# Performance work log

Measured on AMD Instinct MI355X. Metric: run time of the kernel, lower is better.

The kernel has to match this reference:

```python
import jax, jax.numpy as jnp
import numpy as np

N_NODES = 100000

def spmm(rows, cols, vals, x):
    # out[r] = sum_e vals[e] * x[cols[e]] for edges with rows[e] == r
    msgs = vals[:, None] * x[cols]            # [E, F]
    return jax.ops.segment_sum(msgs, rows, num_segments=N_NODES)

def setup_inputs() -> dict:
    key = jax.random.key(0)
    ks = jax.random.split(key, 8)
    N, E, F_IN, H, C = N_NODES, 1600000, 128, 128, 64
    x = jax.random.normal(ks[0], (N, F_IN), dtype=jnp.float32)
    edge_rows = jax.random.randint(ks[1], (E,), 0, N, dtype=jnp.int32)
    edge_cols = jax.random.randint(ks[2], (E,), 0, N, dtype=jnp.int32)
    edge_vals = jax.random.uniform(ks[3], (E,), dtype=jnp.float32)
    W1 = jax.random.normal(ks[4], (F_IN, H), dtype=jnp.float32) * (1.0 / np.sqrt(F_IN))
    b1 = jnp.zeros((H,), dtype=jnp.float32)
    W2 = jax.random.normal(ks[5], (H, C), dtype=jnp.float32) * (1.0 / np.sqrt(H))
    b2 = jnp.zeros((C,), dtype=jnp.float32)
    return {"x": x, "edge_rows": edge_rows, "edge_cols": edge_cols,
            "edge_vals": edge_vals, "W1": W1, "b1": b1, "W2": W2, "b2": b2}

def reference(x, edge_rows, edge_cols, edge_vals, W1, b1, W2, b2):
    # Layer 1: spmm(adj, x) then linear, then ReLU (dropout = identity at eval)
    h = spmm(edge_rows, edge_cols, edge_vals, x)   # [N, F_IN]
    h = h @ W1 + b1                                # [N, H]
    h = jax.nn.relu(h)
    # Layer 2
    h = spmm(edge_rows, edge_cols, edge_vals, h)   # [N, H]
    return h @ W2 + b2                             # [N, C]
```

## Files before the change

### kernel.cpp

```cpp
#include <hip/hip_runtime.h>


typedef __attribute__((ext_vector_type(8))) short short8;
typedef __attribute__((ext_vector_type(4))) float floatx4;
typedef __attribute__((ext_vector_type(2))) float floatx2;

#define ELLS 64
#define H2LD 136
#define RW   256
#define CH   4096
#define EPT  16
#define MAXB 400

static __device__ __forceinline__ unsigned short f2bf(float f) {
    unsigned int u = __builtin_bit_cast(unsigned int, f);
    u += 0x7fffu + ((u >> 16) & 1u);
    return (unsigned short)(u >> 16);
}
static __device__ __forceinline__ float bflo(unsigned int u) {
    return __builtin_bit_cast(float, u << 16);
}
static __device__ __forceinline__ float bfhi(unsigned int u) {
    return __builtin_bit_cast(float, u & 0xffff0000u);
}
static __device__ __forceinline__ float slotval(unsigned int s) {
    return (float)(s >> 17) * (1.0f / 32767.0f);
}

__global__ __launch_bounds__(256) void prep_kernel(
    const float* __restrict__ W1, const float* __restrict__ W2,
    unsigned short* __restrict__ W1t, unsigned short* __restrict__ W2t)
{
    int idx = blockIdx.x * 256 + threadIdx.x;
    if (idx < 128 * 128) {
        int n = idx >> 7, k = idx & 127;
        W1t[idx] = f2bf(W1[(size_t)k * 128 + n]);
    }
    if (idx < 64 * 128) {
        int n = idx >> 7, k = idx & 127;
        W2t[idx] = f2bf(W2[(size_t)k * 64 + n]);
    }
}

static __device__ __forceinline__ void gemm1_body(
    const float* __restrict__ A, const unsigned short* __restrict__ Wt,
    unsigned short* __restrict__ Y, int N, int bid)
{
    const int lane = threadIdx.x & 63;
    const int wave = threadIdx.x >> 6;
    const int quad = lane >> 4;
    const int l16  = lane & 15;
    const int row0 = bid * 64 + wave * 16;
    int arow = row0 + l16;
    if (arow > N - 1) arow = N - 1;

    short8 af[4];
    const float* ap = A + (size_t)arow * 128 + quad * 8;
    #pragma unroll
    for (int kt = 0; kt < 4; ++kt) {
        const floatx4* p = (const floatx4*)(ap + kt * 32);
        floatx4 lo = __builtin_nontemporal_load(p);
        floatx4 hi = __builtin_nontemporal_load(p + 1);
        short8 t;
        t[0] = (short)f2bf(lo[0]); t[1] = (short)f2bf(lo[1]);
        t[2] = (short)f2bf(lo[2]); t[3] = (short)f2bf(lo[3]);
        t[4] = (short)f2bf(hi[0]); t[5] = (short)f2bf(hi[1]);
        t[6] = (short)f2bf(hi[2]); t[7] = (short)f2bf(hi[3]);
        af[kt] = t;
    }

    floatx4 acc[8];
    #pragma unroll
    for (int nt = 0; nt < 8; ++nt) acc[nt] = (floatx4){0.f, 0.f, 0.f, 0.f};

    #pragma unroll
    for (int nt = 0; nt < 8; ++nt) {
        const unsigned short* wp = Wt + (size_t)(nt * 16 + l16) * 128 + quad * 8;
        #pragma unroll
        for (int kt = 0; kt < 4; ++kt) {
            short8 bfr = *(const short8*)(wp + kt * 32);
            acc[nt] = __builtin_amdgcn_mfma_f32_16x16x32_bf16(
                af[kt], bfr, acc[nt], 0, 0, 0);
        }
    }

    #pragma unroll
    for (int nt = 0; nt < 8; ++nt) {
        int col = nt * 16 + l16;
        #pragma unroll
        for (int r = 0; r < 4; ++r) {
            int row = row0 + quad * 4 + r;
            if (row < N)
                Y[(size_t)row * 128 + col] = f2bf(acc[nt][r]);
        }
    }
}

__global__ __launch_bounds__(256) void binA_gemm1_fused(
    const int* __restrict__ erow, const int* __restrict__ ecol,
    const float* __restrict__ eval,
    uint2* __restrict__ slab, unsigned int* __restrict__ offsT,
    int E, int NC, int NB,
    const float* __restrict__ x, const unsigned short* __restrict__ W1t,
    unsigned short* __restrict__ y1b, int N)
{
    __shared__ unsigned int hist[MAXB + 1];
    __shared__ uint2 compact[CH];

    if ((int)blockIdx.x < NC) {
        const int t     = threadIdx.x;
        const int chunk = blockIdx.x;

        for (int i = t; i <= NB; i += 256) hist[i] = 0;
        __syncthreads();

        int base = chunk * CH + t * EPT;
        unsigned int w0[EPT];
        unsigned int vb[EPT];
        int bk[EPT], rk[EPT];

        if (base + EPT <= E) {
            #pragma unroll
            for (int q = 0; q < 4; ++q) {
                int4   r4 = *(const int4*)(erow + base + q * 4);
                int4   c4 = *(const int4*)(ecol + base + q * 4);
                float4 v4 = *(const float4*)(eval + base + q * 4);
                int rr[4]   = {r4.x, r4.y, r4.z, r4.w};
                int cc[4]   = {c4.x, c4.y, c4.z, c4.w};
                float vv[4] = {v4.x, v4.y, v4.z, v4.w};
                #pragma unroll
                for (int j = 0; j < 4; ++j) {
                    int i = q * 4 + j;
                    bk[i] = rr[j] >> 8;
                    w0[i] = (unsigned int)cc[j]
                          | (((unsigned int)rr[j] & (RW - 1)) << 17);
                    vb[i] = __builtin_bit_cast(unsigned int, vv[j]);
                }
            }
        } else {
            #pragma unroll
            for (int j = 0; j < EPT; ++j) {
                int e = base + j;
                if (e < E) {
                    int r = erow[e];
                    bk[j] = r >> 8;
                    w0[j] = (unsigned int)ecol[e]
                          | (((unsigned int)r & (RW - 1)) << 17);
                    vb[j] = __builtin_bit_cast(unsigned int, eval[e]);
                } else {
                    bk[j] = NB;
                    w0[j] = 0u; vb[j] = 0u;
                }
            }
        }

        #pragma unroll
        for (int j = 0; j < EPT; ++j)
            rk[j] = (int)atomicAdd(&hist[bk[j]], 1u);
        __syncthreads();

        if (t == 0) {
            unsigned int run = 0;
            for (int i = 0; i <= NB; ++i) {
                unsigned int c = hist[i];
                hist[i] = run;
                run += c;
            }
        }
        __syncthreads();

        #pragma unroll
        for (int j = 0; j < EPT; ++j) {
            unsigned int pos = hist[bk[j]] + (unsigned int)rk[j];
            uint2 e; e.x = w0[j]; e.y = vb[j];
            compact[pos] = e;
        }
        __syncthreads();

        uint2* sp = slab + (size_t)chunk * CH;
        #pragma unroll
        for (int s = 0; s < EPT; ++s)
            sp[s * 256 + t] = compact[s * 256 + t];
        unsigned int* op = offsT + (size_t)chunk * (NB + 1);
        for (int i = t; i <= NB; i += 256) op[i] = hist[i];
    } else {
        gemm1_body(x, W1t, y1b, N, blockIdx.x - NC);
    }
}

__global__ __launch_bounds__(256) void binB(
    const uint2* __restrict__ slab, const unsigned int* __restrict__ offsT,
    unsigned int* __restrict__ ell, int* __restrict__ deg,
    int NC, int NB, int N)
{
    __shared__ unsigned int ell_lds[RW * ELLS];
    __shared__ unsigned int cur[RW];

    const int t = threadIdx.x;
    const int b = blockIdx.x;

    for (int i = t; i < RW; i += 256) cur[i] = 0;
    __syncthreads();

    const int grp = t >> 5;
    const int sl  = t & 31;
    for (int cbase = 0; cbase < NC; cbase += 8) {
        int c = cbase + grp;
        if (c < NC) {
            const unsigned int* op = offsT + (size_t)c * (NB + 1) + b;
            unsigned int off = op[0];
            unsigned int end = op[1];
            const uint2* sp = slab + (size_t)c * CH;
            for (unsigned int i = off + (unsigned)sl; i < end; i += 32) {
                uint2 e = sp[i];
                unsigned int rin = e.x >> 17;
                unsigned int col = e.x & 0x1FFFFu;
                float v = __builtin_bit_cast(float, e.y);
                unsigned int q = (unsigned int)(int)(v * 32767.f + 0.5f);
                unsigned int p = atomicAdd(&cur[rin], 1u);
                if (p < ELLS)
                    ell_lds[rin * ELLS + p] = col | (q << 17);
            }
        }
    }
    __syncthreads();

    const uint4* src = (const uint4*)ell_lds;
    uint4* dst = (uint4*)(ell + (size_t)b * RW * ELLS);
    #pragma unroll
    for (int s = 0; s < (RW * ELLS / 4) / 256; ++s)
        dst[s * 256 + t] = src[s * 256 + t];

    int row = b * RW + t;
    if (row < N) deg[row] = min((int)cur[t], ELLS);
}

__global__ __launch_bounds__(1024, 8) void spmm128_gemm2_fused(
    const int* __restrict__ deg, const unsigned int* __restrict__ ell,
    const unsigned short* __restrict__ y1b, const float* __restrict__ b1,
    const unsigned short* __restrict__ W2t,
    unsigned short* __restrict__ y2b, int N)
{
    __shared__ unsigned short h2s[16 * H2LD];

    const int wave = threadIdx.x >> 6;
    const int lane = threadIdx.x & 63;
    const int row  = blockIdx.x * 16 + wave;

    unsigned int pack = 0;
    if (row < N) {
        const unsigned int* xf = (const unsigned int*)y1b;
        int d  = min(deg[row], ELLS);
        int d8 = (d + 7) & ~7;
        const unsigned int* ep = ell + ((size_t)row << 6);

        float ax[8], ay[8];
        #pragma unroll
        for (int j = 0; j < 8; ++j) { ax[j] = 0.f; ay[j] = 0.f; }

        for (int i = 0; i < d8; i += 8) {
            uint4 q0 = *(const uint4*)(ep + i);
            uint4 q1 = *(const uint4*)(ep + i + 4);
            unsigned int s[8] = {q0.x, q0.y, q0.z, q0.w,
                                 q1.x, q1.y, q1.z, q1.w};
            unsigned int sv[8];
            unsigned int u[8];
            #pragma unroll
            for (int j = 0; j < 8; ++j) {
                unsigned int ss = (i + j < d) ? s[j] : 0u;
                sv[j] = ss;
                u[j] = xf[((ss & 0x1FFFFu) << 6) | (unsigned)lane];
            }
            #pragma unroll
            for (int j = 0; j < 8; ++j) {
                float vvv = slotval(sv[j]);
                ax[j] = fmaf(vvv, bflo(u[j]), ax[j]);
                ay[j] = fmaf(vvv, bfhi(u[j]), ay[j]);
            }
        }
        float2 b = ((const float2*)b1)[lane];
        float sx = ((ax[0] + ax[1]) + (ax[2] + ax[3]))
                 + ((ax[4] + ax[5]) + (ax[6] + ax[7])) + b.x;
        float sy = ((ay[0] + ay[1]) + (ay[2] + ay[3]))
                 + ((ay[4] + ay[5]) + (ay[6] + ay[7])) + b.y;
        sx = fmaxf(sx, 0.f);
        sy = fmaxf(sy, 0.f);
        pack = (unsigned int)f2bf(sx) | ((unsigned int)f2bf(sy) << 16);
    }
    ((unsigned int*)(h2s + wave * H2LD))[lane] = pack;
    __syncthreads();

    if (wave < 4) {
        const int quad = lane >> 4;
        const int l16  = lane & 15;
        const int nt   = wave;

        short8 af[4];
        #pragma unroll
        for (int kt = 0; kt < 4; ++kt)
            af[kt] = *(const short8*)(h2s + l16 * H2LD + quad * 8 + kt * 32);

        floatx4 acc = (floatx4){0.f, 0.f, 0.f, 0.f};
        const unsigned short* wp = W2t + (size_t)(nt * 16 + l16) * 128 + quad * 8;
        #pragma unroll
        for (int kt = 0; kt < 4; ++kt) {
            short8 bfr = *(const short8*)(wp + kt * 32);
            acc = __builtin_amdgcn_mfma_f32_16x16x32_bf16(af[kt], bfr, acc, 0, 0, 0);
        }

        int col = nt * 16 + l16;
        #pragma unroll
        for (int r = 0; r < 4; ++r) {
            int grow = blockIdx.x * 16 + quad * 4 + r;
            if (grow < N)
                y2b[(size_t)grow * 64 + col] = f2bf(acc[r]);
        }
    }
}

__global__ __launch_bounds__(256) void spmm_gather64_out(
    const int* __restrict__ deg, const unsigned int* __restrict__ ell,
    const unsigned short* __restrict__ y2b,
    const float* __restrict__ bias, float* __restrict__ out, int N)
{
    int row = (blockIdx.x * 256 + threadIdx.x) >> 6;
    if (row >= N) return;
    int lane = threadIdx.x & 63;
    int half = lane >> 5, fl = lane & 31;
    const unsigned int* xf = (const unsigned int*)y2b;

    int d  = min(deg[row], ELLS);
    int d8 = (d + 7) & ~7;
    const unsigned int* ep = ell + ((size_t)row << 6);

    float ax[4], ay[4];
    #pragma unroll
    for (int j = 0; j < 4; ++j) { ax[j] = 0.f; ay[j] = 0.f; }

    for (int i = half * 4; i < d8; i += 8) {
        uint4 q = *(const uint4*)(ep + i);
        unsigned int s[4] = {q.x, q.y, q.z, q.w};
        unsigned int sv[4];
        unsigned int u[4];
        #pragma unroll
        for (int j = 0; j < 4; ++j) {
            unsigned int ss = (i + j < d) ? s[j] : 0u;
            sv[j] = ss;
            u[j] = xf[((ss & 0x1FFFFu) << 5) | (unsigned)fl];
        }
        #pragma unroll
        for (int j = 0; j < 4; ++j) {
            float vvv = slotval(sv[j]);
            ax[j] = fmaf(vvv, bflo(u[j]), ax[j]);
            ay[j] = fmaf(vvv, bfhi(u[j]), ay[j]);
        }
    }
    float sx = (ax[0] + ax[1]) + (ax[2] + ax[3]);
    float sy = (ay[0] + ay[1]) + (ay[2] + ay[3]);
    sx += __shfl_xor(sx, 32);
    sy += __shfl_xor(sy, 32);
    if (half == 0) {
        float2 b = ((const float2*)bias)[fl];
        floatx2 o; o[0] = sx + b.x; o[1] = sy + b.y;
        __builtin_nontemporal_store(o, (floatx2*)out + (size_t)row * 32 + fl);
    }
}

extern "C" void kernel_launch(void* const* d_in, const int* in_sizes, int n_in,
                              void* d_out, int out_size, void* d_ws, size_t ws_size,
                              hipStream_t stream)
{
    const float* x    = (const float*)d_in[0];
    const int*   erow = (const int*)  d_in[1];
    const int*   ecol = (const int*)  d_in[2];
    const float* eval = (const float*)d_in[3];
    const float* W1   = (const float*)d_in[4];
    const float* b1   = (const float*)d_in[5];
    const float* W2   = (const float*)d_in[6];
    const float* b2   = (const float*)d_in[7];
    float*       out  = (float*)d_out;

    const int N = in_sizes[0] / 128;
    const int E = in_sizes[1];
    const int NP = N + 64;
    const int NB = (N + RW - 1) / RW;
    const int NC = (E + CH - 1) / CH;

    unsigned short* y1b = (unsigned short*)d_ws;
    unsigned short* y2b = y1b + (size_t)NP * 128;
    unsigned short* W1t = y2b + (size_t)NP * 64;
    unsigned short* W2t = W1t + 128 * 128;
    unsigned int* ell   = (unsigned int*)(W2t + 64 * 128);
    uint2* slab         = (uint2*)(ell + (size_t)NB * RW * ELLS);
    unsigned int* offsT = (unsigned int*)(slab + (size_t)NC * CH);
    int* deg            = (int*)(offsT + (size_t)NC * (NB + 1));

    const int spmm_blocks  = (N + 3) / 4;
    const int fused_blocks = (N + 15) / 16;
    const int mfma_blocks  = (N + 63) / 64;
    const int prep_blocks  = (128 * 128 + 255) / 256;

    prep_kernel<<<prep_blocks, 256, 0, stream>>>(W1, W2, W1t, W2t);

    binA_gemm1_fused<<<NC + mfma_blocks, 256, 0, stream>>>(
        erow, ecol, eval, slab, offsT, E, NC, NB, x, W1t, y1b, N);

    binB<<<NB, 256, 0, stream>>>(slab, offsT, ell, deg, NC, NB, N);

    spmm128_gemm2_fused<<<fused_blocks, 1024, 0, stream>>>(
        deg, ell, y1b, b1, W2t, y2b, N);

    spmm_gather64_out<<<spmm_blocks, 256, 0, stream>>>(
        deg, ell, y2b, b2, out, N);
}
```

Baseline: 299.8 us.

## Slice feature matrices into 16-column panels for cache-local SpMM gathers

Stores the intermediate feature matrices in a column-sliced layout (16 bf16 columns per slice, 32 bytes per row) and splits each SpMM across slices, so each block gathers from one small panel that fits better in L2/MALL. The fused spmm+gemm2 kernel is replaced by a sliced SpMM that writes h2 to memory, a separate MFMA gemm2 kernel, and a sliced output SpMM. Edge slots are loaded once per wave and broadcast with ds_bpermute. In exchange, h2 makes an extra round trip through global memory, there is one more launch, and each gather fetches only 32 bytes per edge.

New measurement: 523.3 us. 74.6% more time.

```diff
diff --git a/kernel.cpp b/kernel.cpp
--- a/kernel.cpp
+++ b/kernel.cpp
@@ -6,7 +6,6 @@
 typedef __attribute__((ext_vector_type(2))) float floatx2;
 
 #define ELLS 64
-#define H2LD 136
 #define RW   256
 #define CH   4096
 #define EPT  16
@@ -44,7 +43,7 @@
 
 static __device__ __forceinline__ void gemm1_body(
     const float* __restrict__ A, const unsigned short* __restrict__ Wt,
-    unsigned short* __restrict__ Y, int N, int bid)
+    unsigned short* __restrict__ Ys, int NP, int N, int bid)
 {
     const int lane = threadIdx.x & 63;
     const int wave = threadIdx.x >> 6;
@@ -86,12 +85,12 @@
 
     #pragma unroll
     for (int nt = 0; nt < 8; ++nt) {
-        int col = nt * 16 + l16;
         #pragma unroll
         for (int r = 0; r < 4; ++r) {
             int row = row0 + quad * 4 + r;
             if (row < N)
-                Y[(size_t)row * 128 + col] = f2bf(acc[nt][r]);
+                Ys[(size_t)nt * NP * 16 + (size_t)row * 16 + l16] =
+                    f2bf(acc[nt][r]);
         }
     }
 }
@@ -102,7 +101,7 @@
     uint2* __restrict__ slab, unsigned int* __restrict__ offsT,
     int E, int NC, int NB,
     const float* __restrict__ x, const unsigned short* __restrict__ W1t,
-    unsigned short* __restrict__ y1b, int N)
+    unsigned short* __restrict__ y1s, int NP, int N)
 {
     __shared__ unsigned int hist[MAXB + 1];
     __shared__ uint2 compact[CH];
@@ -184,7 +183,7 @@
         unsigned int* op = offsT + (size_t)chunk * (NB + 1);
         for (int i = t; i <= NB; i += 256) op[i] = hist[i];
     } else {
-        gemm1_body(x, W1t, y1b, N, blockIdx.x - NC);
+        gemm1_body(x, W1t, y1s, NP, N, blockIdx.x - NC);
     }
 }
 
@@ -235,134 +234,139 @@
     if (row < N) deg[row] = min((int)cur[t], ELLS);
 }
 
-__global__ __launch_bounds__(1024, 8) void spmm128_gemm2_fused(
+__global__ __launch_bounds__(1024) void spmm1_sliced(
     const int* __restrict__ deg, const unsigned int* __restrict__ ell,
-    const unsigned short* __restrict__ y1b, const float* __restrict__ b1,
+    const unsigned short* __restrict__ y1s, const float* __restrict__ b1,
+    unsigned short* __restrict__ h2s, int NP, int N)
+{
+    const int slice = blockIdx.x & 7;
+    const int rblk  = blockIdx.x >> 3;
+    const int wave  = threadIdx.x >> 6;
+    const int lane  = threadIdx.x & 63;
+    const int j     = lane >> 3;
+    const int sl    = lane & 7;
+    const int row   = rblk * 16 + wave;
+    if (row >= N) return;
+
+    const unsigned int* xu = (const unsigned int*)y1s + (size_t)slice * NP * 8;
+    const unsigned int* ep = ell + ((size_t)row << 6);
+    const int d = deg[row];
+
+    unsigned int myslot = (lane < d) ? ep[lane] : 0u;
+
+    float ax = 0.f, ay = 0.f;
+    for (int i = 0; i < d; i += 8) {
+        int src = i + j;
+        unsigned int w = (unsigned int)__builtin_amdgcn_ds_bpermute(
+            src << 2, (int)myslot);
+        w = (src < d) ? w : 0u;
+        unsigned int u = xu[(w & 0x1FFFFu) * 8 + (unsigned)sl];
+        float v = slotval(w);
+        ax = fmaf(v, bflo(u), ax);
+        ay = fmaf(v, bfhi(u), ay);
+    }
+    ax += __shfl_xor(ax, 8);  ay += __shfl_xor(ay, 8);
+    ax += __shfl_xor(ax, 16); ay += __shfl_xor(ay, 16);
+    ax += __shfl_xor(ax, 32); ay += __shfl_xor(ay, 32);
+
+    if (j == 0) {
+        float2 b = ((const float2*)b1)[slice * 8 + sl];
+        float sx = fmaxf(ax + b.x, 0.f);
+        float sy = fmaxf(ay + b.y, 0.f);
+        unsigned int pk = (unsigned int)f2bf(sx)
+                        | ((unsigned int)f2bf(sy) << 16);
+        ((unsigned int*)h2s)[(size_t)slice * NP * 8 + (size_t)row * 8 + sl] = pk;
+    }
+}
+
+__global__ __launch_bounds__(256) void gemm2_kernel(
+    const unsigned short* __restrict__ h2s,
     const unsigned short* __restrict__ W2t,
-    unsigned short* __restrict__ y2b, int N)
-{
-    __shared__ unsigned short h2s[16 * H2LD];
-
+    unsigned short* __restrict__ y2s, int NP, int N)
+{
+    const int lane = threadIdx.x & 63;
     const int wave = threadIdx.x >> 6;
-    const int lane = threadIdx.x & 63;
-    const int row  = blockIdx.x * 16 + wave;
-
-    unsigned int pack = 0;
-    if (row < N) {
-        const unsigned int* xf = (const unsigned int*)y1b;
-        int d  = min(deg[row], ELLS);
-        int d8 = (d + 7) & ~7;
-        const unsigned int* ep = ell + ((size_t)row << 6);
-
-        float ax[8], ay[8];
-        #pragma unroll
-        for (int j = 0; j < 8; ++j) { ax[j] = 0.f; ay[j] = 0.f; }
-
-        for (int i = 0; i < d8; i += 8) {
-            uint4 q0 = *(const uint4*)(ep + i);
-            uint4 q1 = *(const uint4*)(ep + i + 4);
-            unsigned int s[8] = {q0.x, q0.y, q0.z, q0.w,
-                                 q1.x, q1.y, q1.z, q1.w};
-            unsigned int sv[8];
-            unsigned int u[8];
-            #pragma unroll
-            for (int j = 0; j < 8; ++j) {
-                unsigned int ss = (i + j < d) ? s[j] : 0u;
-                sv[j] = ss;
-                u[j] = xf[((ss & 0x1FFFFu) << 6) | (unsigned)lane];
-            }
-            #pragma unroll
-            for (int j = 0; j < 8; ++j) {
-                float vvv = slotval(sv[j]);
-                ax[j] = fmaf(vvv, bflo(u[j]), ax[j]);
-                ay[j] = fmaf(vvv, bfhi(u[j]), ay[j]);
-            }
-        }
-        float2 b = ((const float2*)b1)[lane];
-        float sx = ((ax[0] + ax[1]) + (ax[2] + ax[3]))
-                 + ((ax[4] + ax[5]) + (ax[6] + ax[7])) + b.x;
-        float sy = ((ay[0] + ay[1]) + (ay[2] + ay[3]))
-                 + ((ay[4] + ay[5]) + (ay[6] + ay[7])) + b.y;
-        sx = fmaxf(sx, 0.f);
-        sy = fmaxf(sy, 0.f);
-        pack = (unsigned int)f2bf(sx) | ((unsigned int)f2bf(sy) << 16);
-    }
-    ((unsigned int*)(h2s + wave * H2LD))[lane] = pack;
-    __syncthreads();
-
-    if (wave < 4) {
-        const int quad = lane >> 4;
-        const int l16  = lane & 15;
-        const int nt   = wave;
-
-        short8 af[4];
-        #pragma unroll
-        for (int kt = 0; kt < 4; ++kt)
-            af[kt] = *(const short8*)(h2s + l16 * H2LD + quad * 8 + kt * 32);
-
-        floatx4 acc = (floatx4){0.f, 0.f, 0.f, 0.f};
+    const int quad = lane >> 4;
+    const int l16  = lane & 15;
+    const int row0 = blockIdx.x * 64 + wave * 16;
+    int arow = row0 + l16;
+    if (arow > N - 1) arow = N - 1;
+
+    short8 af[4];
+    #pragma unroll
+    for (int kt = 0; kt < 4; ++kt) {
+        int slice = kt * 2 + (quad >> 1);
+        af[kt] = *(const short8*)(h2s + (size_t)slice * NP * 16
+                                  + (size_t)arow * 16 + (quad & 1) * 8);
+    }
+
+    floatx4 acc[4];
+    #pragma unroll
+    for (int nt = 0; nt < 4; ++nt) acc[nt] = (floatx4){0.f, 0.f, 0.f, 0.f};
+
+    #pragma unroll
+    for (int nt = 0; nt < 4; ++nt) {
         const unsigned short* wp = W2t + (size_t)(nt * 16 + l16) * 128 + quad * 8;
         #pragma unroll
         for (int kt = 0; kt < 4; ++kt) {
             short8 bfr = *(const short8*)(wp + kt * 32);
-            acc = __builtin_amdgcn_mfma_f32_16x16x32_bf16(af[kt], bfr, acc, 0, 0, 0);
-        }
-
-        int col = nt * 16 + l16;
+            acc[nt] = __builtin_amdgcn_mfma_f32_16x16x32_bf16(
+                af[kt], bfr, acc[nt], 0, 0, 0);
+        }
+    }
+
+    #pragma unroll
+    for (int nt = 0; nt < 4; ++nt) {
         #pragma unroll
         for (int r = 0; r < 4; ++r) {
-            int grow = blockIdx.x * 16 + quad * 4 + r;
-            if (grow < N)
-                y2b[(size_t)grow * 64 + col] = f2bf(acc[r]);
-        }
-    }
-}
-
-__global__ __launch_bounds__(256) void spmm_gather64_out(
+            int row = row0 + quad * 4 + r;
+            if (row < N)
+                y2s[(size_t)nt * NP * 16 + (size_t)row * 16 + l16] =
+                    f2bf(acc[nt][r]);
+        }
+    }
+}
+
+__global__ __launch_bounds__(1024) void spmm2_sliced(
     const int* __restrict__ deg, const unsigned int* __restrict__ ell,
-    const unsigned short* __restrict__ y2b,
-    const float* __restrict__ bias, float* __restrict__ out, int N)
-{
-    int row = (blockIdx.x * 256 + threadIdx.x) >> 6;
+    const unsigned short* __restrict__ y2s, const float* __restrict__ b2,
+    float* __restrict__ out, int NP, int N)
+{
+    const int slice = blockIdx.x & 3;
+    const int rblk  = blockIdx.x >> 2;
+    const int wave  = threadIdx.x >> 6;
+    const int lane  = threadIdx.x & 63;
+    const int j     = lane >> 3;
+    const int sl    = lane & 7;
+    const int row   = rblk * 16 + wave;
     if (row >= N) return;
-    int lane = threadIdx.x & 63;
-    int half = lane >> 5, fl = lane & 31;
-    const unsigned int* xf = (const unsigned int*)y2b;
-
-    int d  = min(deg[row], ELLS);
-    int d8 = (d + 7) & ~7;
+
+    const unsigned int* xu = (const unsigned int*)y2s + (size_t)slice * NP * 8;
     const unsigned int* ep = ell + ((size_t)row << 6);
-
-    float ax[4], ay[4];
-    #pragma unroll
-    for (int j = 0; j < 4; ++j) { ax[j] = 0.f; ay[j] = 0.f; }
-
-    for (int i = half * 4; i < d8; i += 8) {
-        uint4 q = *(const uint4*)(ep + i);
-        unsigned int s[4] = {q.x, q.y, q.z, q.w};
-        unsigned int sv[4];
-        unsigned int u[4];
-        #pragma unroll
-        for (int j = 0; j < 4; ++j) {
-            unsigned int ss = (i + j < d) ? s[j] : 0u;
-            sv[j] = ss;
-            u[j] = xf[((ss & 0x1FFFFu) << 5) | (unsigned)fl];
-        }
-        #pragma unroll
-        for (int j = 0; j < 4; ++j) {
-            float vvv = slotval(sv[j]);
-            ax[j] = fmaf(vvv, bflo(u[j]), ax[j]);
-            ay[j] = fmaf(vvv, bfhi(u[j]), ay[j]);
-        }
-    }
-    float sx = (ax[0] + ax[1]) + (ax[2] + ax[3]);
-    float sy = (ay[0] + ay[1]) + (ay[2] + ay[3]);
-    sx += __shfl_xor(sx, 32);
-    sy += __shfl_xor(sy, 32);
-    if (half == 0) {
-        float2 b = ((const float2*)bias)[fl];
-        floatx2 o; o[0] = sx + b.x; o[1] = sy + b.y;
-        __builtin_nontemporal_store(o, (floatx2*)out + (size_t)row * 32 + fl);
+    const int d = deg[row];
+
+    unsigned int myslot = (lane < d) ? ep[lane] : 0u;
+
+    float ax = 0.f, ay = 0.f;
+    for (int i = 0; i < d; i += 8) {
+        int src = i + j;
+        unsigned int w = (unsigned int)__builtin_amdgcn_ds_bpermute(
+            src << 2, (int)myslot);
+        w = (src < d) ? w : 0u;
+        unsigned int u = xu[(w & 0x1FFFFu) * 8 + (unsigned)sl];
+        float v = slotval(w);
+        ax = fmaf(v, bflo(u), ax);
+        ay = fmaf(v, bfhi(u), ay);
+    }
+    ax += __shfl_xor(ax, 8);  ay += __shfl_xor(ay, 8);
+    ax += __shfl_xor(ax, 16); ay += __shfl_xor(ay, 16);
+    ax += __shfl_xor(ax, 32); ay += __shfl_xor(ay, 32);
+
+    if (j == 0) {
+        float2 b = ((const float2*)b2)[slice * 8 + sl];
+        floatx2 o; o[0] = ax + b.x; o[1] = ay + b.y;
+        __builtin_nontemporal_store(
+            o, (floatx2*)out + (size_t)row * 32 + slice * 8 + sl);
     }
 }
 
@@ -386,30 +390,33 @@
     const int NB = (N + RW - 1) / RW;
     const int NC = (E + CH - 1) / CH;
 
-    unsigned short* y1b = (unsigned short*)d_ws;
-    unsigned short* y2b = y1b + (size_t)NP * 128;
-    unsigned short* W1t = y2b + (size_t)NP * 64;
+    unsigned short* y1s = (unsigned short*)d_ws;
+    unsigned short* h2s = y1s + (size_t)NP * 128;
+    unsigned short* W1t = h2s + (size_t)NP * 128;
     unsigned short* W2t = W1t + 128 * 128;
     unsigned int* ell   = (unsigned int*)(W2t + 64 * 128);
     uint2* slab         = (uint2*)(ell + (size_t)NB * RW * ELLS);
     unsigned int* offsT = (unsigned int*)(slab + (size_t)NC * CH);
     int* deg            = (int*)(offsT + (size_t)NC * (NB + 1));
-
-    const int spmm_blocks  = (N + 3) / 4;
-    const int fused_blocks = (N + 15) / 16;
+    unsigned short* y2s = (unsigned short*)slab;
+
     const int mfma_blocks  = (N + 63) / 64;
     const int prep_blocks  = (128 * 128 + 255) / 256;
+    const int s1_blocks    = ((N + 15) / 16) * 8;
+    const int s2_blocks    = ((N + 15) / 16) * 4;
 
     prep_kernel<<<prep_blocks, 256, 0, stream>>>(W1, W2, W1t, W2t);
 
     binA_gemm1_fused<<<NC + mfma_blocks, 256, 0, stream>>>(
-        erow, ecol, eval, slab, offsT, E, NC, NB, x, W1t, y1b, N);
+        erow, ecol, eval, slab, offsT, E, NC, NB, x, W1t, y1s, NP, N);
 
     binB<<<NB, 256, 0, stream>>>(slab, offsT, ell, deg, NC, NB, N);
 
-    spmm128_gemm2_fused<<<fused_blocks, 1024, 0, stream>>>(
-        deg, ell, y1b, b1, W2t, y2b, N);
-
-    spmm_gather64_out<<<spmm_blocks, 256, 0, stream>>>(
-        deg, ell, y2b, b2, out, N);
-}
+    spmm1_sliced<<<s1_blocks, 1024, 0, stream>>>(
+        deg, ell, y1s, b1, h2s, NP, N);
+
+    gemm2_kernel<<<mfma_blocks, 256, 0, stream>>>(h2s, W2t, y2s, NP, N);
+
+    spmm2_sliced<<<s2_blocks, 1024, 0, stream>>>(
+        deg, ell, y2s, b2, out, NP, N);
+}
```
